# Performance work log

Hardware: AMD Instinct MI355X
Metric: run time of the kernel (lower is better)

The kernel has to match this reference:

```python
import jax, jax.numpy as jnp
import numpy as np

V = 128          # vocab_size
S = 32           # sentence_size
E = 16           # embedding_size
M = 128          # memory_size
L = 128          # linear_output_size
B = 16
N = 127


def _position_encoding(sentence_size, embedding_size):
    enc = np.ones((embedding_size, sentence_size), dtype=np.float32)
    ls = sentence_size + 1
    le = embedding_size + 1
    for i in range(1, le):
        for j in range(1, ls):
            enc[i - 1, j - 1] = (i - (le - 1) / 2) * (j - (ls - 1) / 2)
    enc = 1 + 4 * enc / embedding_size / sentence_size
    return enc.T  # [S, E]


def setup_inputs() -> dict:
    key = jax.random.key(0)
    ks = jax.random.split(key, 12)
    node_fts = jax.random.randint(ks[0], (B, N, S), 0, V).astype(jnp.float32)
    edge_fts = jax.random.randint(ks[1], (B, N, N, S), 0, V).astype(jnp.float32)
    graph_fts = jax.random.randint(ks[2], (B, S), 0, V).astype(jnp.float32)
    adj_mat = jax.random.randint(ks[3], (B, N, N), 0, 2).astype(jnp.float32)
    hidden = jnp.zeros((B, N, E), jnp.float32)
    sc = 0.02
    query_biases = sc * jax.random.normal(ks[4], (V - 1, E), jnp.float32)
    stories_biases = sc * jax.random.normal(ks[5], (V - 1, E), jnp.float32)
    output_biases = sc * jax.random.normal(ks[6], (V - 1, E), jnp.float32)
    memory_contents = sc * jax.random.normal(ks[7], (M, E), jnp.float32)
    W_int = sc * jax.random.normal(ks[8], (E, E), jnp.float32)   # intermediate_linear (unused, num_hops=1)
    W_out = sc * jax.random.normal(ks[9], (E, L), jnp.float32)   # output_linear
    W_fin = sc * jax.random.normal(ks[10], (L, V), jnp.float32)  # final_linear
    enc = jnp.asarray(_position_encoding(S, E))
    return dict(node_fts=node_fts, edge_fts=edge_fts, graph_fts=graph_fts,
                adj_mat=adj_mat, hidden=hidden, enc=enc,
                query_biases=query_biases, stories_biases=stories_biases,
                output_biases=output_biases, memory_contents=memory_contents,
                W_int=W_int, W_out=W_out, W_fin=W_fin)


def reference(node_fts, edge_fts, graph_fts, adj_mat, hidden, enc,
              query_biases, stories_biases, output_biases, memory_contents,
              W_int, W_out, W_fin):
    del hidden
    b, n, s = node_fts.shape
    # [B, N+1, S]: nodes plus graph feature row
    naf = jnp.concatenate([node_fts, graph_fts[:, None, :]], axis=1)
    # mask edges then pad to [B, N+1, N+1, S]
    ef = edge_fts * adj_mat[..., None]
    ef = jnp.pad(ef, ((0, 0), (0, 1), (0, 1), (0, 0)))
    bt = b * (n + 1)
    queries = naf.reshape(bt, s)                 # [BT, S]
    stories = ef.reshape(bt, n + 1, s)           # [BT, M0, S], M0 = N+1

    nil = jnp.zeros((1, enc.shape[1]), queries.dtype)
    sb = jnp.concatenate([stories_biases, nil], axis=0)   # [V, E]
    qb = jnp.concatenate([query_biases, nil], axis=0)
    ob = jnp.concatenate([output_biases, nil], axis=0)

    sidx = jnp.maximum(stories.astype(jnp.int32), 0)       # clamp_min(0)
    qidx = jnp.maximum(queries.astype(jnp.int32), 0)

    # position-encoded weighted sums over the sentence axis
    mem = jnp.einsum('bmse,se->bme', sb[sidx], enc)        # [BT, M0, E]
    Cj = jnp.einsum('bmse,se->bme', ob[sidx], enc)         # [BT, M0, E]
    pad_m = memory_contents.shape[0] - (n + 1)
    mem = jnp.pad(mem, ((0, 0), (0, pad_m), (0, 0))) + memory_contents
    Cj = jnp.pad(Cj, ((0, 0), (0, pad_m), (0, 0)))
    u = jnp.einsum('bse,se->be', qb[qidx], enc)            # [BT, E]

    # num_hops = 1
    x = u
    probs = jax.nn.softmax(jnp.einsum('bme,be->bm', mem, x), axis=-1)
    o = jnp.einsum('bme,bm->be', Cj, probs)
    x = jax.nn.relu((x + o) @ W_out)                       # last hop -> output_linear + relu
    ret = x @ W_fin                                        # [BT, V]

    nxt = ret.reshape(b, n + 1, -1)
    return nxt[:, :-1, :] + nxt[:, -1:, :]                 # [B, N, V]
```

## Files before the change

### kernel.cpp

```cpp
#include <hip/hip_runtime.h>

#define Vn 128
#define Sn 32
#define En 16
#define M0 128
#define Ln 128
#define Bn 16
#define Nn 127
#define NROWS (Bn * Nn)
#define RS 20
#define CE(e) (((float)(e) - 7.0f) * 0.0078125f)
#define ESUM(e) (32.f + 16.f * CE(e))
#define WS_UO 0
#define WS_UG 32768
#define WS_CC 33024

__global__ __launch_bounds__(256, 8) void memnet_core(
    const float* __restrict__ node_fts, const float* __restrict__ edge_fts,
    const float* __restrict__ graph_fts, const float* __restrict__ adjm,
    const float* __restrict__ qb, const float* __restrict__ sb,
    const float* __restrict__ ob, const float* __restrict__ mc,
    float* __restrict__ ws)
{
    __shared__ __align__(16) float sbL[M0 * RS];
    __shared__ unsigned int idxw[M0 * 8];
    __shared__ float scoresL[M0];
    __shared__ float uL[En];
    __shared__ float ugL[En];
    __shared__ float cM[En];
    __shared__ float cC[En];
    __shared__ float owaveL[4 * En];
    __shared__ int listL[128];
    __shared__ int flagL[128];
    __shared__ int wcnt[2];

    const int t = threadIdx.x;
    const int bt = blockIdx.x;
    const int b = bt / 127;
    const int lane = t & 63;
    const int wv = t >> 6;

    for (int c = t; c < 512; c += 256) {
        int r = c >> 2, q = c & 3;
        float4 v = make_float4(0.f, 0.f, 0.f, 0.f);
        if (r < 127) v = *(const float4*)&sb[r * 16 + q * 4];
        *(float4*)&sbL[r * RS + q * 4] = v;
    }
    if (t < 128) {
        bool flag = (t < 127) && (adjm[(size_t)bt * 127 + t] != 0.f);
        unsigned long long msk = __ballot(flag);
        int pos = (int)__popcll(msk & ((1ull << lane) - 1ull));
        if (flag) listL[(t & 64) + pos] = t;
        if (lane == 0) wcnt[t >> 6] = (int)__popcll(msk);
        flagL[t] = flag ? 1 : 0;
    }
    for (int c = t; c < 1024; c += 256) {
        int m = c >> 3, q = c & 7;
        if (m < 127 && adjm[(size_t)bt * 127 + m] != 0.f) {
            float4 v = *(const float4*)&edge_fts[(size_t)(bt * 127 + m) * 32 + q * 4];
            idxw[m * 8 + q] = (unsigned)(int)v.x | ((unsigned)(int)v.y << 8)
                            | ((unsigned)(int)v.z << 16) | ((unsigned)(int)v.w << 24);
        }
    }
    {
        const int e = lane & 15, sg = lane >> 4;
        if (wv == 0 || wv == 2) {
            const float* qsrc = (wv == 0) ? &node_fts[(size_t)bt * 32]
                                          : &graph_fts[b * 32];
            float q0 = 0.f, q1 = 0.f;
#pragma unroll
            for (int k = 0; k < 8; k++) {
                int s = sg + 4 * k;
                int qi = (int)qsrc[s];
                if (qi < 0) qi = 0;
                float w = (qi < 127) ? qb[qi * 16 + e] : 0.f;
                q0 += w;
                q1 = fmaf((float)s - 15.0f, w, q1);
            }
            q0 += __shfl_xor(q0, 16); q0 += __shfl_xor(q0, 32);
            q1 += __shfl_xor(q1, 16); q1 += __shfl_xor(q1, 32);
            if (lane < 16) {
                float ue = fmaf(CE(e), q1, q0);
                if (wv == 0) uL[e] = ue; else ugL[e] = ue;
            }
        } else if (wv == 1 && lane < 16) {
            cM[e] = sb[e] * ESUM(e);
            cC[e] = ob[e] * ESUM(e);
        }
    }
    __syncthreads();

    if (t < 128 && !flagL[t]) {
        float p = 0.f;
#pragma unroll
        for (int e4 = 0; e4 < 16; e4 += 4) {
            float4 m4 = *(const float4*)&mc[t * 16 + e4];
            p = fmaf(cM[e4 + 0] + m4.x, uL[e4 + 0], p);
            p = fmaf(cM[e4 + 1] + m4.y, uL[e4 + 1], p);
            p = fmaf(cM[e4 + 2] + m4.z, uL[e4 + 2], p);
            p = fmaf(cM[e4 + 3] + m4.w, uL[e4 + 3], p);
        }
        scoresL[t] = p;
    }

    const int eg4 = (t & 3) * 4;
    const int qd = t >> 2;
    const int c0 = wcnt[0];
    const int nact = c0 + wcnt[1];
    const float4 u4 = *(const float4*)&uL[eg4];
    const float4 ce = make_float4(CE(eg4), CE(eg4 + 1), CE(eg4 + 2), CE(eg4 + 3));

    float4 aC_A = make_float4(0.f, 0.f, 0.f, 0.f);
    float4 aC_B = make_float4(0.f, 0.f, 0.f, 0.f);
    int mA = -1, mB = -1;

    if (qd < nact) {
        mA = listL[(qd < c0) ? qd : (qd - c0 + 64)];
        float4 aM = make_float4(0.f, 0.f, 0.f, 0.f);
        for (int sq = 0; sq < 8; sq++) {
            unsigned w0 = idxw[mA * 8 + sq];
            float sfb = (float)(sq * 4) - 15.0f;
#pragma unroll
            for (int j = 0; j < 4; j++) {
                int i0 = (w0 >> (8 * j)) & 0xFF;
                int i0c = (i0 < 127) ? i0 : 126;
                float sf = sfb + (float)j;
                float4 ef = make_float4(fmaf(ce.x, sf, 1.f), fmaf(ce.y, sf, 1.f),
                                        fmaf(ce.z, sf, 1.f), fmaf(ce.w, sf, 1.f));
                float4 a0 = *(const float4*)&sbL[i0 * RS + eg4];
                float4 cv = *(const float4*)&ob[i0c * 16 + eg4];
                if (i0 == 127) cv = make_float4(0.f, 0.f, 0.f, 0.f);
                aM.x = fmaf(a0.x, ef.x, aM.x); aM.y = fmaf(a0.y, ef.y, aM.y);
                aM.z = fmaf(a0.z, ef.z, aM.z); aM.w = fmaf(a0.w, ef.w, aM.w);
                aC_A.x = fmaf(cv.x, ef.x, aC_A.x); aC_A.y = fmaf(cv.y, ef.y, aC_A.y);
                aC_A.z = fmaf(cv.z, ef.z, aC_A.z); aC_A.w = fmaf(cv.w, ef.w, aC_A.w);
            }
        }
        float4 mc4 = *(const float4*)&mc[mA * 16 + eg4];
        float p = (aM.x + mc4.x) * u4.x + (aM.y + mc4.y) * u4.y
                + (aM.z + mc4.z) * u4.z + (aM.w + mc4.w) * u4.w;
        p += __shfl_xor(p, 1); p += __shfl_xor(p, 2);
        if ((t & 3) == 0) scoresL[mA] = p;
    }
    if (qd + 64 < nact) {
        int g = qd + 64;
        mB = listL[(g < c0) ? g : (g - c0 + 64)];
        float4 aM = make_float4(0.f, 0.f, 0.f, 0.f);
        for (int sq = 0; sq < 8; sq++) {
            unsigned w0 = idxw[mB * 8 + sq];
            float sfb = (float)(sq * 4) - 15.0f;
#pragma unroll
            for (int j = 0; j < 4; j++) {
                int i0 = (w0 >> (8 * j)) & 0xFF;
                int i0c = (i0 < 127) ? i0 : 126;
                float sf = sfb + (float)j;
                float4 ef = make_float4(fmaf(ce.x, sf, 1.f), fmaf(ce.y, sf, 1.f),
                                        fmaf(ce.z, sf, 1.f), fmaf(ce.w, sf, 1.f));
                float4 a0 = *(const float4*)&sbL[i0 * RS + eg4];
                float4 cv = *(const float4*)&ob[i0c * 16 + eg4];
                if (i0 == 127) cv = make_float4(0.f, 0.f, 0.f, 0.f);
                aM.x = fmaf(a0.x, ef.x, aM.x); aM.y = fmaf(a0.y, ef.y, aM.y);
                aM.z = fmaf(a0.z, ef.z, aM.z); aM.w = fmaf(a0.w, ef.w, aM.w);
                aC_B.x = fmaf(cv.x, ef.x, aC_B.x); aC_B.y = fmaf(cv.y, ef.y, aC_B.y);
                aC_B.z = fmaf(cv.z, ef.z, aC_B.z); aC_B.w = fmaf(cv.w, ef.w, aC_B.w);
            }
        }
        float4 mc4 = *(const float4*)&mc[mB * 16 + eg4];
        float p = (aM.x + mc4.x) * u4.x + (aM.y + mc4.y) * u4.y
                + (aM.z + mc4.z) * u4.z + (aM.w + mc4.w) * u4.w;
        p += __shfl_xor(p, 1); p += __shfl_xor(p, 2);
        if ((t & 3) == 0) scoresL[mB] = p;
    }
    __syncthreads();

    float pmask;
    {
        float v1 = scoresL[lane], v2 = scoresL[lane + 64];
        int f1 = flagL[lane], f2 = flagL[lane + 64];
        float mv = fmaxf(v1, v2);
#pragma unroll
        for (int off = 32; off > 0; off >>= 1) mv = fmaxf(mv, __shfl_xor(mv, off));
        float e1 = __expf(v1 - mv), e2 = __expf(v2 - mv);
        float sv = e1 + e2;
        float sm = (f1 ? 0.f : e1) + (f2 ? 0.f : e2);
#pragma unroll
        for (int off = 32; off > 0; off >>= 1) {
            sv += __shfl_xor(sv, off);
            sm += __shfl_xor(sm, off);
        }
        pmask = sm / sv;

        float4 op = make_float4(0.f, 0.f, 0.f, 0.f);
        if (mA >= 0) {
            float pa = __expf(scoresL[mA] - mv) / sv;
            op.x = pa * aC_A.x; op.y = pa * aC_A.y;
            op.z = pa * aC_A.z; op.w = pa * aC_A.w;
        }
        if (mB >= 0) {
            float pb = __expf(scoresL[mB] - mv) / sv;
            op.x = fmaf(pb, aC_B.x, op.x); op.y = fmaf(pb, aC_B.y, op.y);
            op.z = fmaf(pb, aC_B.z, op.z); op.w = fmaf(pb, aC_B.w, op.w);
        }
#pragma unroll
        for (int off = 4; off <= 32; off <<= 1) {
            op.x += __shfl_xor(op.x, off);
            op.y += __shfl_xor(op.y, off);
            op.z += __shfl_xor(op.z, off);
            op.w += __shfl_xor(op.w, off);
        }
        if (lane < 4) *(float4*)&owaveL[wv * 16 + lane * 4] = op;
    }
    __syncthreads();

    if (t < 16) {
        float o = owaveL[t] + owaveL[16 + t] + owaveL[32 + t] + owaveL[48 + t];
        ws[WS_UO + bt * 16 + t] = uL[t] + o + cC[t] * pmask;
        if (bt % 127 == 0) ws[WS_UG + b * 16 + t] = ugL[t];
        if (bt == 0) ws[WS_CC + t] = cC[t];
    }
}

__global__ __launch_bounds__(256, 8) void memnet_tail(
    const float* __restrict__ ws, const float* __restrict__ wout,
    const float* __restrict__ wfin, float* __restrict__ out)
{
    __shared__ __align__(16) float woutL[16 * 128];
    __shared__ float xsum[16][130];
    __shared__ float uoT[16][16];
    __shared__ float xgV[128];
    __shared__ float ugcc[16];

    const int t = threadIdx.x;
    const int b = blockIdx.x >> 3;
    const int c = blockIdx.x & 7;
    const int i0 = c * 16;

    {
        const float4* src = (const float4*)wout;
        float4* dst = (float4*)woutL;
        dst[t] = src[t];
        dst[t + 256] = src[t + 256];
    }
    {
        int r = t >> 4, e = t & 15;
        int i = i0 + r;
        uoT[r][e] = (i < 127) ? ws[WS_UO + (size_t)(b * 127 + i) * 16 + e] : 0.f;
        if (t < 16) ugcc[t] = ws[WS_UG + b * 16 + t] + ws[WS_CC + t];
    }
    __syncthreads();
    if (t < 128) {
        float acc = 0.f;
#pragma unroll
        for (int e = 0; e < 16; e++) acc = fmaf(ugcc[e], woutL[e * 128 + t], acc);
        xgV[t] = fmaxf(acc, 0.f);
    }
    __syncthreads();
    {
        int r = t >> 4;
#pragma unroll
        for (int k = 0; k < 8; k++) {
            int l = (t & 15) + 16 * k;
            float acc = 0.f;
#pragma unroll
            for (int e = 0; e < 16; e++) acc = fmaf(uoT[r][e], woutL[e * 128 + l], acc);
            xsum[r][l] = fmaxf(acc, 0.f) + xgV[l];
        }
    }
    __syncthreads();
    {
        int r = t >> 4, v0 = (t & 15) * 8;
        int i = i0 + r;
        float acc[8] = {0.f, 0.f, 0.f, 0.f, 0.f, 0.f, 0.f, 0.f};
        for (int l = 0; l < 128; l++) {
            float s = xsum[r][l];
            const float4 w0 = *(const float4*)&wfin[l * 128 + v0];
            const float4 w1 = *(const float4*)&wfin[l * 128 + v0 + 4];
            acc[0] = fmaf(s, w0.x, acc[0]); acc[1] = fmaf(s, w0.y, acc[1]);
            acc[2] = fmaf(s, w0.z, acc[2]); acc[3] = fmaf(s, w0.w, acc[3]);
            acc[4] = fmaf(s, w1.x, acc[4]); acc[5] = fmaf(s, w1.y, acc[5]);
            acc[6] = fmaf(s, w1.z, acc[6]); acc[7] = fmaf(s, w1.w, acc[7]);
        }
        if (i < 127) {
            float4* o0 = (float4*)&out[((size_t)(b * 127 + i)) * 128 + v0];
            o0[0] = make_float4(acc[0], acc[1], acc[2], acc[3]);
            o0[1] = make_float4(acc[4], acc[5], acc[6], acc[7]);
        }
    }
}

extern "C" void kernel_launch(void* const* d_in, const int* in_sizes, int n_in,
                              void* d_out, int out_size, void* d_ws, size_t ws_size,
                              hipStream_t stream)
{
    const float* node  = (const float*)d_in[0];
    const float* edge  = (const float*)d_in[1];
    const float* graph = (const float*)d_in[2];
    const float* adjm  = (const float*)d_in[3];
    const float* qb    = (const float*)d_in[6];
    const float* sb    = (const float*)d_in[7];
    const float* ob    = (const float*)d_in[8];
    const float* mc    = (const float*)d_in[9];
    const float* wout  = (const float*)d_in[11];
    const float* wfin  = (const float*)d_in[12];

    float* ws = (float*)d_ws;

    memnet_core<<<NROWS, 256, 0, stream>>>(node, edge, graph, adjm, qb,
                                           sb, ob, mc, ws);
    memnet_tail<<<Bn * 8, 256, 0, stream>>>(ws, wout, wfin, (float*)d_out);
}
```

Baseline: 142.2 us.

## Factor position-encoded memory scores through per-vocab projections and probability histograms

```diff
diff --git a/kernel.cpp b/kernel.cpp
--- a/kernel.cpp
+++ b/kernel.cpp
@@ -8,7 +8,6 @@
 #define Bn 16
 #define Nn 127
 #define NROWS (Bn * Nn)
-#define RS 20
 #define CE(e) (((float)(e) - 7.0f) * 0.0078125f)
 #define ESUM(e) (32.f + 16.f * CE(e))
 #define WS_UO 0
@@ -22,14 +21,15 @@
     const float* __restrict__ ob, const float* __restrict__ mc,
     float* __restrict__ ws)
 {
-    __shared__ __align__(16) float sbL[M0 * RS];
     __shared__ unsigned int idxw[M0 * 8];
+    __shared__ float2 suV[128];
     __shared__ float scoresL[M0];
+    __shared__ float probsL[M0];
+    __shared__ float g0[128], g1[128];
     __shared__ float uL[En];
     __shared__ float ugL[En];
     __shared__ float cM[En];
     __shared__ float cC[En];
-    __shared__ float owaveL[4 * En];
     __shared__ int listL[128];
     __shared__ int flagL[128];
     __shared__ int wcnt[2];
@@ -40,12 +40,7 @@
     const int lane = t & 63;
     const int wv = t >> 6;
 
-    for (int c = t; c < 512; c += 256) {
-        int r = c >> 2, q = c & 3;
-        float4 v = make_float4(0.f, 0.f, 0.f, 0.f);
-        if (r < 127) v = *(const float4*)&sb[r * 16 + q * 4];
-        *(float4*)&sbL[r * RS + q * 4] = v;
-    }
+    if (t < 128) { g0[t] = 0.f; g1[t] = 0.f; }
     if (t < 128) {
         bool flag = (t < 127) && (adjm[(size_t)bt * 127 + t] != 0.f);
         unsigned long long msk = __ballot(flag);
@@ -90,86 +85,60 @@
     }
     __syncthreads();
 
-    if (t < 128 && !flagL[t]) {
-        float p = 0.f;
-#pragma unroll
-        for (int e4 = 0; e4 < 16; e4 += 4) {
-            float4 m4 = *(const float4*)&mc[t * 16 + e4];
-            p = fmaf(cM[e4 + 0] + m4.x, uL[e4 + 0], p);
-            p = fmaf(cM[e4 + 1] + m4.y, uL[e4 + 1], p);
-            p = fmaf(cM[e4 + 2] + m4.z, uL[e4 + 2], p);
-            p = fmaf(cM[e4 + 3] + m4.w, uL[e4 + 3], p);
-        }
-        scoresL[t] = p;
-    }
-
-    const int eg4 = (t & 3) * 4;
-    const int qd = t >> 2;
+    if (t < 128) {
+        float s0 = 0.f, s1 = 0.f;
+        if (t < 127) {
+            const float4* rp = (const float4*)&sb[t * 16];
+#pragma unroll
+            for (int q = 0; q < 4; q++) {
+                float4 r = rp[q];
+                float4 uu = *(const float4*)&uL[q * 4];
+                int e0 = q * 4;
+                s0 += r.x * uu.x + r.y * uu.y + r.z * uu.z + r.w * uu.w;
+                s1 += CE(e0) * r.x * uu.x + CE(e0 + 1) * r.y * uu.y
+                    + CE(e0 + 2) * r.z * uu.z + CE(e0 + 3) * r.w * uu.w;
+            }
+        }
+        suV[t] = make_float2(s0, s1);
+    } else {
+        int m = t - 128;
+        const float4* mp = (const float4*)&mc[m * 16];
+        float mcu = 0.f, cMu = 0.f;
+#pragma unroll
+        for (int q = 0; q < 4; q++) {
+            float4 mm = mp[q];
+            float4 uu = *(const float4*)&uL[q * 4];
+            float4 cm = *(const float4*)&cM[q * 4];
+            mcu += mm.x * uu.x + mm.y * uu.y + mm.z * uu.z + mm.w * uu.w;
+            cMu += cm.x * uu.x + cm.y * uu.y + cm.z * uu.z + cm.w * uu.w;
+        }
+        scoresL[m] = mcu + (flagL[m] ? 0.f : cMu);
+    }
+    __syncthreads();
+
+    const int g = t >> 1;
     const int c0 = wcnt[0];
     const int nact = c0 + wcnt[1];
-    const float4 u4 = *(const float4*)&uL[eg4];
-    const float4 ce = make_float4(CE(eg4), CE(eg4 + 1), CE(eg4 + 2), CE(eg4 + 3));
-
-    float4 aC_A = make_float4(0.f, 0.f, 0.f, 0.f);
-    float4 aC_B = make_float4(0.f, 0.f, 0.f, 0.f);
-    int mA = -1, mB = -1;
-
-    if (qd < nact) {
-        mA = listL[(qd < c0) ? qd : (qd - c0 + 64)];
-        float4 aM = make_float4(0.f, 0.f, 0.f, 0.f);
-        for (int sq = 0; sq < 8; sq++) {
-            unsigned w0 = idxw[mA * 8 + sq];
-            float sfb = (float)(sq * 4) - 15.0f;
+    unsigned wreg[4];
+    int mS = -1;
+    if (g < nact) {
+        mS = listL[(g < c0) ? g : (g - c0 + 64)];
+        const int sh = t & 1;
+        float acc = 0.f;
+#pragma unroll
+        for (int k = 0; k < 4; k++) {
+            unsigned w = idxw[mS * 8 + sh * 4 + k];
+            wreg[k] = w;
+            float sbase = (float)(sh * 16 + k * 4) - 15.0f;
 #pragma unroll
             for (int j = 0; j < 4; j++) {
-                int i0 = (w0 >> (8 * j)) & 0xFF;
-                int i0c = (i0 < 127) ? i0 : 126;
-                float sf = sfb + (float)j;
-                float4 ef = make_float4(fmaf(ce.x, sf, 1.f), fmaf(ce.y, sf, 1.f),
-                                        fmaf(ce.z, sf, 1.f), fmaf(ce.w, sf, 1.f));
-                float4 a0 = *(const float4*)&sbL[i0 * RS + eg4];
-                float4 cv = *(const float4*)&ob[i0c * 16 + eg4];
-                if (i0 == 127) cv = make_float4(0.f, 0.f, 0.f, 0.f);
-                aM.x = fmaf(a0.x, ef.x, aM.x); aM.y = fmaf(a0.y, ef.y, aM.y);
-                aM.z = fmaf(a0.z, ef.z, aM.z); aM.w = fmaf(a0.w, ef.w, aM.w);
-                aC_A.x = fmaf(cv.x, ef.x, aC_A.x); aC_A.y = fmaf(cv.y, ef.y, aC_A.y);
-                aC_A.z = fmaf(cv.z, ef.z, aC_A.z); aC_A.w = fmaf(cv.w, ef.w, aC_A.w);
-            }
-        }
-        float4 mc4 = *(const float4*)&mc[mA * 16 + eg4];
-        float p = (aM.x + mc4.x) * u4.x + (aM.y + mc4.y) * u4.y
-                + (aM.z + mc4.z) * u4.z + (aM.w + mc4.w) * u4.w;
-        p += __shfl_xor(p, 1); p += __shfl_xor(p, 2);
-        if ((t & 3) == 0) scoresL[mA] = p;
-    }
-    if (qd + 64 < nact) {
-        int g = qd + 64;
-        mB = listL[(g < c0) ? g : (g - c0 + 64)];
-        float4 aM = make_float4(0.f, 0.f, 0.f, 0.f);
-        for (int sq = 0; sq < 8; sq++) {
-            unsigned w0 = idxw[mB * 8 + sq];
-            float sfb = (float)(sq * 4) - 15.0f;
-#pragma unroll
-            for (int j = 0; j < 4; j++) {
-                int i0 = (w0 >> (8 * j)) & 0xFF;
-                int i0c = (i0 < 127) ? i0 : 126;
-                float sf = sfb + (float)j;
-                float4 ef = make_float4(fmaf(ce.x, sf, 1.f), fmaf(ce.y, sf, 1.f),
-                                        fmaf(ce.z, sf, 1.f), fmaf(ce.w, sf, 1.f));
-                float4 a0 = *(const float4*)&sbL[i0 * RS + eg4];
-                float4 cv = *(const float4*)&ob[i0c * 16 + eg4];
-                if (i0 == 127) cv = make_float4(0.f, 0.f, 0.f, 0.f);
-                aM.x = fmaf(a0.x, ef.x, aM.x); aM.y = fmaf(a0.y, ef.y, aM.y);
-                aM.z = fmaf(a0.z, ef.z, aM.z); aM.w = fmaf(a0.w, ef.w, aM.w);
-                aC_B.x = fmaf(cv.x, ef.x, aC_B.x); aC_B.y = fmaf(cv.y, ef.y, aC_B.y);
-                aC_B.z = fmaf(cv.z, ef.z, aC_B.z); aC_B.w = fmaf(cv.w, ef.w, aC_B.w);
-            }
-        }
-        float4 mc4 = *(const float4*)&mc[mB * 16 + eg4];
-        float p = (aM.x + mc4.x) * u4.x + (aM.y + mc4.y) * u4.y
-                + (aM.z + mc4.z) * u4.z + (aM.w + mc4.w) * u4.w;
-        p += __shfl_xor(p, 1); p += __shfl_xor(p, 2);
-        if ((t & 3) == 0) scoresL[mB] = p;
+                int i = (w >> (8 * j)) & 255;
+                float2 sv2 = suV[i];
+                acc += sv2.x + (sbase + (float)j) * sv2.y;
+            }
+        }
+        acc += __shfl_xor(acc, 1);
+        if ((t & 1) == 0) scoresL[mS] += acc;
     }
     __syncthreads();
 
@@ -189,34 +158,49 @@
             sm += __shfl_xor(sm, off);
         }
         pmask = sm / sv;
-
-        float4 op = make_float4(0.f, 0.f, 0.f, 0.f);
-        if (mA >= 0) {
-            float pa = __expf(scoresL[mA] - mv) / sv;
-            op.x = pa * aC_A.x; op.y = pa * aC_A.y;
-            op.z = pa * aC_A.z; op.w = pa * aC_A.w;
-        }
-        if (mB >= 0) {
-            float pb = __expf(scoresL[mB] - mv) / sv;
-            op.x = fmaf(pb, aC_B.x, op.x); op.y = fmaf(pb, aC_B.y, op.y);
-            op.z = fmaf(pb, aC_B.z, op.z); op.w = fmaf(pb, aC_B.w, op.w);
-        }
-#pragma unroll
-        for (int off = 4; off <= 32; off <<= 1) {
-            op.x += __shfl_xor(op.x, off);
-            op.y += __shfl_xor(op.y, off);
-            op.z += __shfl_xor(op.z, off);
-            op.w += __shfl_xor(op.w, off);
-        }
-        if (lane < 4) *(float4*)&owaveL[wv * 16 + lane * 4] = op;
-    }
-    __syncthreads();
-
-    if (t < 16) {
-        float o = owaveL[t] + owaveL[16 + t] + owaveL[32 + t] + owaveL[48 + t];
-        ws[WS_UO + bt * 16 + t] = uL[t] + o + cC[t] * pmask;
-        if (bt % 127 == 0) ws[WS_UG + b * 16 + t] = ugL[t];
-        if (bt == 0) ws[WS_CC + t] = cC[t];
+        if (wv == 0) {
+            float inv = 1.f / sv;
+            probsL[lane] = e1 * inv;
+            probsL[lane + 64] = e2 * inv;
+        }
+    }
+    __syncthreads();
+
+    if (mS >= 0) {
+        float p = probsL[mS];
+        const int sh = t & 1;
+#pragma unroll
+        for (int k = 0; k < 4; k++) {
+            unsigned w = wreg[k];
+            float sbase = (float)(sh * 16 + k * 4) - 15.0f;
+#pragma unroll
+            for (int j = 0; j < 4; j++) {
+                int i = (w >> (8 * j)) & 255;
+                atomicAdd(&g0[i], p);
+                atomicAdd(&g1[i], p * (sbase + (float)j));
+            }
+        }
+    }
+    __syncthreads();
+
+    if (wv == 0) {
+        const int e = lane & 15, vq = lane >> 4;
+        const float cee = CE(e);
+        float acc = 0.f;
+        for (int k = 0; k < 32; k++) {
+            int v = vq + 4 * k;
+            if (v < 127)
+                acc = fmaf(fmaf(cee, g1[v], g0[v]), ob[v * 16 + e], acc);
+        }
+        acc += __shfl_xor(acc, 16);
+        acc += __shfl_xor(acc, 32);
+        if (lane < 16) {
+            float uo = uL[e] + acc + cC[e] * pmask;
+            ws[WS_UO + bt * 16 + e] = uo;
+        }
+    } else if (wv == 1 && lane < 16) {
+        if (bt % 127 == 0) ws[WS_UG + b * 16 + lane] = ugL[lane];
+        if (bt == 0) ws[WS_CC + lane] = cC[lane];
     }
 }
 
```

Measured after the change: 162.7 us. 1.14x slower.
